# Performance work log

Hardware: AMD Instinct MI355X
Metric: run time of the kernel (lower is better)

Reference implementation:

```python
import jax, jax.numpy as jnp
import numpy as np


def crf_log_likelihood(logits, tags, mask, transitions, start_trans, end_trans):
    """AllenNLP-style linear-chain CRF log-likelihood, summed over the batch.
    logits: [B,T,K] float, tags: [B,T] int, mask: [B,T] float (1=valid).
    include_start_end_transitions=True.
    """
    B, T, K = logits.shape
    lt = jnp.transpose(logits, (1, 0, 2))          # [T,B,K]
    mt = jnp.transpose(mask, (1, 0))               # [T,B]
    tt = jnp.transpose(tags, (1, 0))               # [T,B]

    # ---- partition function (forward algorithm) ----
    alpha0 = start_trans + lt[0]                   # [B,K]

    def part_step(alpha, xs):
        emit, m = xs                               # emit [B,K], m [B]
        # inner[b,i,j] = alpha[b,i] + transitions[i,j] + emit[b,j]
        inner = alpha[:, :, None] + emit[:, None, :] + transitions[None, :, :]
        new_alpha = jax.nn.logsumexp(inner, axis=1)
        alpha = new_alpha * m[:, None] + alpha * (1.0 - m[:, None])
        return alpha, None

    alpha, _ = jax.lax.scan(part_step, alpha0, (lt[1:], mt[1:]))
    log_denominator = jax.nn.logsumexp(alpha + end_trans, axis=1)  # [B]

    # ---- joint (gold-path) score ----
    score0 = start_trans[tt[0]]                    # [B]

    def joint_step(score, xs):
        cur, nxt, emit, m_cur, m_nxt = xs
        trans_s = transitions[cur, nxt]                                   # [B]
        emit_s = jnp.take_along_axis(emit, cur[:, None], axis=1)[:, 0]    # [B]
        return score + trans_s * m_nxt + emit_s * m_cur, None

    score, _ = jax.lax.scan(joint_step, score0,
                            (tt[:-1], tt[1:], lt[:-1], mt[:-1], mt[1:]))
    last_idx = (jnp.sum(mt, axis=0) - 1.0).astype(jnp.int32)              # [B]
    last_tags = tt[last_idx, jnp.arange(B)]                               # [B]
    last_emit = jnp.take_along_axis(lt[-1], last_tags[:, None], axis=1)[:, 0]
    score = score + end_trans[last_tags] + last_emit * mt[-1]
    return jnp.sum(score - log_denominator)


def setup_inputs() -> dict:
    key = jax.random.key(0)
    ks = jax.random.split(key, 6)
    B, T, D, K = 64, 512, 768, 21
    vectors = jax.random.normal(ks[0], (B, T, D), dtype=jnp.float32)
    targets = jax.random.randint(ks[1], (B, T), 0, K, dtype=jnp.int32)
    mask = jnp.ones((B, T), dtype=jnp.int32)
    # Linear(input_dim, n_classes)
    W = jax.random.normal(ks[2], (K, D), dtype=jnp.float32) * (1.0 / np.sqrt(D))
    b = jax.random.normal(ks[3], (K,), dtype=jnp.float32) * 0.01
    transitions = jax.random.normal(ks[4], (K, K), dtype=jnp.float32) * 0.1
    se = jax.random.normal(ks[5], (2, K), dtype=jnp.float32) * 0.1
    return {"vectors": vectors, "targets": targets, "mask": mask,
            "W": W, "b": b, "transitions": transitions,
            "start_trans": se[0], "end_trans": se[1]}


def reference(vectors, targets, mask, W, b, transitions, start_trans, end_trans):
    logits = jnp.einsum('btd,kd->btk', vectors, W) + b     # proj
    maskf = mask.astype(logits.dtype)
    ll = crf_log_likelihood(logits, targets, maskf, transitions, start_trans, end_trans)
    loss = -ll / jnp.sum(maskf)
    return loss, logits
```

## Files before the change

### kernel.cpp

```cpp
#include <hip/hip_runtime.h>

#define B_ 64
#define T_ 512
#define D_ 768
#define K_ 21
#define NCHUNK 32
#define CLEN 16
#define GSTRIDE 448
#define LOG21 3.0445224377234229965f

using f16x8 = __attribute__((ext_vector_type(8))) _Float16;
using f32x4 = __attribute__((ext_vector_type(4))) float;

__global__ __launch_bounds__(256) void proj_kernel(
    const float* __restrict__ A,
    const float* __restrict__ W,
    const float* __restrict__ bias,
    float* __restrict__ out)
{
    const int lane = threadIdx.x & 63;
    const int wave = threadIdx.x >> 6;
    const int row0 = (blockIdx.x * 4 + wave) * 16;
    const int m = lane & 15;
    const int kb = (lane >> 4) * 8;

    const float* __restrict__ Ar  = A + (size_t)(row0 + m) * D_ + kb;
    const float* __restrict__ Wr0 = W + (size_t)m * D_ + kb;
    const int n1 = (16 + m < K_) ? 16 + m : K_ - 1;
    const float* __restrict__ Wr1 = W + (size_t)n1 * D_ + kb;

    f32x4 acc0 = {0.f, 0.f, 0.f, 0.f};
    f32x4 acc1 = {0.f, 0.f, 0.f, 0.f};

    #pragma unroll 8
    for (int s = 0; s < 24; ++s) {
        const float4 aL = *(const float4*)(Ar  + s * 32);
        const float4 aH = *(const float4*)(Ar  + s * 32 + 4);
        const float4 bL = *(const float4*)(Wr0 + s * 32);
        const float4 bH = *(const float4*)(Wr0 + s * 32 + 4);
        const float4 cL = *(const float4*)(Wr1 + s * 32);
        const float4 cH = *(const float4*)(Wr1 + s * 32 + 4);
        f16x8 af, bf, cf;
        af[0]=(_Float16)aL.x; af[1]=(_Float16)aL.y; af[2]=(_Float16)aL.z; af[3]=(_Float16)aL.w;
        af[4]=(_Float16)aH.x; af[5]=(_Float16)aH.y; af[6]=(_Float16)aH.z; af[7]=(_Float16)aH.w;
        bf[0]=(_Float16)bL.x; bf[1]=(_Float16)bL.y; bf[2]=(_Float16)bL.z; bf[3]=(_Float16)bL.w;
        bf[4]=(_Float16)bH.x; bf[5]=(_Float16)bH.y; bf[6]=(_Float16)bH.z; bf[7]=(_Float16)bH.w;
        cf[0]=(_Float16)cL.x; cf[1]=(_Float16)cL.y; cf[2]=(_Float16)cL.z; cf[3]=(_Float16)cL.w;
        cf[4]=(_Float16)cH.x; cf[5]=(_Float16)cH.y; cf[6]=(_Float16)cH.z; cf[7]=(_Float16)cH.w;
        acc0 = __builtin_amdgcn_mfma_f32_16x16x32_f16(af, bf, acc0, 0, 0, 0);
        acc1 = __builtin_amdgcn_mfma_f32_16x16x32_f16(af, cf, acc1, 0, 0, 0);
    }

    const int rbase = row0 + (lane >> 4) * 4;
    {
        const float bb = bias[m];
        float* o = out + 1 + (size_t)rbase * K_ + m;
        #pragma unroll
        for (int r = 0; r < 4; ++r) o[(size_t)r * K_] = acc0[r] + bb;
    }
    const int col2 = 16 + m;
    if (col2 < K_) {
        const float bb = bias[col2];
        float* o = out + 1 + (size_t)rbase * K_ + col2;
        #pragma unroll
        for (int r = 0; r < 4; ++r) o[(size_t)r * K_] = acc1[r] + bb;
    }
}

__global__ __launch_bounds__(64) void chunk_kernel(
    const float* __restrict__ outF,
    const int*   __restrict__ mask,
    const float* __restrict__ trans,
    float* __restrict__ G,
    float* __restrict__ SC)
{
    __shared__ float M0[441], M1[441];
    __shared__ float sET[441];
    __shared__ float em[CLEN * K_];
    __shared__ float smx[CLEN];
    __shared__ int   smask[CLEN];

    const int c = blockIdx.x;
    const int b = blockIdx.y;
    const int lane = threadIdx.x;
    const int t0 = c * CLEN + 1;
    const int nst = min(CLEN, T_ - t0);
    const int i_ = lane / 3;
    const int jg = lane - i_ * 3;
    const bool act = lane < 63;

    const float* lg = outF + 1 + (size_t)b * T_ * K_;
    for (int idx = lane; idx < nst * K_; idx += 64) em[idx] = lg[t0 * K_ + idx];
    if (lane < nst) smask[lane] = mask[b * T_ + t0 + lane];
    for (int idx = lane; idx < 441; idx += 64) {
        M0[idx] = (idx % 22 == 0) ? 1.0f : 0.0f;
        sET[idx] = __expf(trans[idx]);
    }
    __syncthreads();

    if (lane < nst) {
        float mx = -1e30f;
        for (int j = 0; j < K_; ++j) mx = fmaxf(mx, em[lane * K_ + j]);
        smx[lane] = mx;
    }
    __syncthreads();
    for (int idx = lane; idx < nst * K_; idx += 64)
        em[idx] = __expf(em[idx] - smx[idx / K_]) * (1.0f / 21.0f);

    float ETc[K_ * 7];
    if (act) {
        #pragma unroll
        for (int mm = 0; mm < K_; ++mm) {
            #pragma unroll
            for (int q = 0; q < 7; ++q)
                ETc[mm * 7 + q] = sET[mm * K_ + jg * 7 + q];
        }
    }
    __syncthreads();

    int cur = 0;
    for (int s = 0; s < nst; ++s) {
        if (smask[s] != 0) {
            const float* Mr = cur ? M1 : M0;
            float*       Mw = cur ? M0 : M1;
            float facc[7] = {0.f,0.f,0.f,0.f,0.f,0.f,0.f};
            if (act) {
                #pragma unroll
                for (int mm = 0; mm < K_; ++mm) {
                    const float lm = Mr[i_ * K_ + mm];
                    #pragma unroll
                    for (int q = 0; q < 7; ++q)
                        facc[q] = fmaf(lm, ETc[mm * 7 + q], facc[q]);
                }
            }
            __syncthreads();
            if (act) {
                #pragma unroll
                for (int q = 0; q < 7; ++q)
                    Mw[i_ * K_ + jg * 7 + q] = facc[q] * em[s * K_ + jg * 7 + q];
            }
            __syncthreads();
            cur ^= 1;
        }
    }

    float* Gc = G + (size_t)(b * NCHUNK + c) * GSTRIDE;
    const float* Mf = cur ? M1 : M0;
    for (int idx = lane; idx < 441; idx += 64) Gc[idx] = Mf[idx];
    if (lane == 0) {
        float sc = 0.0f;
        for (int s = 0; s < nst; ++s)
            if (smask[s] != 0) sc += smx[s] + LOG21;
        SC[b * NCHUNK + c] = sc;
    }
}

__global__ __launch_bounds__(64) void scan_kernel(
    const float* __restrict__ outF,
    const int*   __restrict__ tags,
    const int*   __restrict__ mask,
    const float* __restrict__ trans,
    const float* __restrict__ startT,
    const float* __restrict__ endT,
    const float* __restrict__ G,
    const float* __restrict__ SC,
    float* __restrict__ ll,
    float* __restrict__ msum)
{
    __shared__ float sG[NCHUNK * GSTRIDE];
    __shared__ float sv[24];
    __shared__ float sm[T_];
    __shared__ int   st[T_];
    const int b = blockIdx.x;
    const int lane = threadIdx.x;
    const int jc = min(lane, K_ - 1);
    const float* lg = outF + 1 + (size_t)b * T_ * K_;
    const float* Gb = G + (size_t)b * NCHUNK * GSTRIDE;

    {
        const float4* Gf4 = (const float4*)Gb;
        float4* dst = (float4*)sG;
        for (int j = lane; j < NCHUNK * GSTRIDE / 4; j += 64) dst[j] = Gf4[j];
    }
    for (int t = lane; t < T_; t += 64) {
        sm[t] = (float)mask[b * T_ + t];
        st[t] = tags[b * T_ + t];
    }
    const float scv = (lane < NCHUNK) ? SC[b * NCHUNK + lane] : 0.0f;

    float val = (lane < K_) ? startT[lane] + lg[lane] : -1e30f;
    float mx = val;
    #pragma unroll
    for (int off = 32; off >= 1; off >>= 1) mx = fmaxf(mx, __shfl_xor(mx, off, 64));
    float v = (lane < K_) ? __expf(val - mx) : 0.0f;
    float C = mx;
    __syncthreads();

    for (int c = 0; c < NCHUNK; ++c) {
        if (lane < K_) sv[lane] = v;
        __syncthreads();
        const float* Gc = sG + c * GSTRIDE;
        float a0 = 0.f, a1 = 0.f, a2 = 0.f;
        #pragma unroll
        for (int i = 0; i < K_; i += 3) {
            a0 = fmaf(sv[i],     Gc[i * K_ + jc],       a0);
            a1 = fmaf(sv[i + 1], Gc[(i + 1) * K_ + jc], a1);
            a2 = fmaf(sv[i + 2], Gc[(i + 2) * K_ + jc], a2);
        }
        const float s = a0 + a1 + a2;
        C += __shfl(scv, c, 64);
        float m2 = (lane < K_) ? s : 0.0f;
        #pragma unroll
        for (int off = 32; off >= 1; off >>= 1) m2 = fmaxf(m2, __shfl_xor(m2, off, 64));
        v = (lane < K_) ? s / m2 : 0.0f;
        C += __logf(m2);
        __syncthreads();
    }

    float term = (lane < K_) ? v * __expf(endT[lane]) : 0.0f;
    #pragma unroll
    for (int off = 32; off >= 1; off >>= 1) term += __shfl_xor(term, off, 64);
    const float logZ = C + __logf(term);

    float sc = 0.0f, ms = 0.0f;
    for (int t = lane; t < T_; t += 64) {
        const float mt = sm[t];
        ms += mt;
        if (t < T_ - 1) {
            const int ct = st[t], nt2 = st[t + 1];
            sc += trans[ct * K_ + nt2] * sm[t + 1] + lg[t * K_ + ct] * mt;
        }
    }
    #pragma unroll
    for (int off = 32; off >= 1; off >>= 1) {
        sc += __shfl_xor(sc, off, 64);
        ms += __shfl_xor(ms, off, 64);
    }
    if (lane == 0) {
        const int lastIdx = (int)ms - 1;
        const int lastTag = st[lastIdx];
        sc += startT[st[0]] + endT[lastTag] + lg[(T_ - 1) * K_ + lastTag] * sm[T_ - 1];
        ll[b]   = sc - logZ;
        msum[b] = ms;
    }
}

__global__ __launch_bounds__(64) void crf_kernel(
    const float* __restrict__ outF,
    const int*   __restrict__ tags,
    const int*   __restrict__ mask,
    const float* __restrict__ trans,
    const float* __restrict__ startT,
    const float* __restrict__ endT,
    float* __restrict__ ws)
{
    __shared__ float se[T_ * K_];
    __shared__ float sm[T_];
    __shared__ int   st[T_];
    const int b = blockIdx.x;
    const int lane = threadIdx.x;

    const float* lg = outF + 1 + (size_t)b * T_ * K_;
    for (int i = lane; i < T_ * K_; i += 64) se[i] = lg[i];
    for (int t = lane; t < T_; t += 64) {
        sm[t] = (float)mask[b * T_ + t];
        st[t] = tags[b * T_ + t];
    }
    __syncthreads();

    const int jc = lane < K_ ? lane : K_ - 1;
    float ET[K_];
    #pragma unroll
    for (int i = 0; i < K_; ++i) ET[i] = __expf(trans[i * K_ + jc]);

    float a0   = startT[jc] + se[jc];
    float r0   = __shfl(a0, 0, 64);
    float aRel = a0 - r0;
    float C    = r0;

    for (int t = 1; t < T_; ++t) {
        if (sm[t] != 0.0f) {
            float e = __expf(aRel);
            float s = 0.0f;
            #pragma unroll
            for (int i = 0; i < K_; ++i)
                s = fmaf(__shfl(e, i, 64), ET[i], s);
            float raw = __logf(s) + se[t * K_ + jc];
            float rr  = __shfl(raw, 0, 64);
            aRel = raw - rr;
            C   += rr;
        }
    }

    float contrib = (lane < K_) ? __expf(aRel + endT[jc]) : 0.0f;
    #pragma unroll
    for (int off = 32; off >= 1; off >>= 1) contrib += __shfl_xor(contrib, off, 64);
    const float logZ = C + __logf(contrib);

    float sc = 0.0f, ms = 0.0f;
    for (int t = lane; t < T_; t += 64) {
        const float mt = sm[t];
        ms += mt;
        if (t < T_ - 1) {
            const int ct = st[t], nt2 = st[t + 1];
            sc += trans[ct * K_ + nt2] * sm[t + 1] + se[t * K_ + ct] * mt;
        }
    }
    #pragma unroll
    for (int off = 32; off >= 1; off >>= 1) {
        sc += __shfl_xor(sc, off, 64);
        ms += __shfl_xor(ms, off, 64);
    }
    if (lane == 0) {
        const int lastIdx = (int)ms - 1;
        const int lastTag = st[lastIdx];
        sc += startT[st[0]] + endT[lastTag] + se[(T_ - 1) * K_ + lastTag] * sm[T_ - 1];
        ws[b]      = sc - logZ;
        ws[B_ + b] = ms;
    }
}

__global__ __launch_bounds__(64) void fin_kernel(
    const float* __restrict__ ll, const float* __restrict__ msum,
    float* __restrict__ outF)
{
    const int lane = threadIdx.x;
    float l = ll[lane];
    float m = msum[lane];
    #pragma unroll
    for (int off = 32; off >= 1; off >>= 1) {
        l += __shfl_xor(l, off, 64);
        m += __shfl_xor(m, off, 64);
    }
    if (lane == 0) outF[0] = -l / m;
}

extern "C" void kernel_launch(void* const* d_in, const int* in_sizes, int n_in,
                              void* d_out, int out_size, void* d_ws, size_t ws_size,
                              hipStream_t stream) {
    const float* A     = (const float*)d_in[0];
    const int*   tags  = (const int*)  d_in[1];
    const int*   mask  = (const int*)  d_in[2];
    const float* W     = (const float*)d_in[3];
    const float* bias  = (const float*)d_in[4];
    const float* trans = (const float*)d_in[5];
    const float* stT   = (const float*)d_in[6];
    const float* enT   = (const float*)d_in[7];
    float* outF = (float*)d_out;
    float* ws   = (float*)d_ws;

    proj_kernel<<<512, 256, 0, stream>>>(A, W, bias, outF);

    const size_t gFloats  = (size_t)B_ * NCHUNK * GSTRIDE;
    const size_t scOff    = gFloats;
    const size_t llOff    = gFloats + (size_t)B_ * NCHUNK;
    const size_t msOff    = llOff + B_;
    const size_t needBytes = (msOff + B_) * sizeof(float);

    if (ws_size >= needBytes) {
        float* G   = ws;
        float* SC  = ws + scOff;
        float* llp = ws + llOff;
        float* msv = ws + msOff;
        chunk_kernel<<<dim3(NCHUNK, B_), 64, 0, stream>>>(outF, mask, trans, G, SC);
        scan_kernel<<<B_, 64, 0, stream>>>(outF, tags, mask, trans, stT, enT, G, SC, llp, msv);
        fin_kernel<<<1, 64, 0, stream>>>(llp, msv, outF);
    } else {
        crf_kernel<<<B_, 64, 0, stream>>>(outF, tags, mask, trans, stT, enT, ws);
        fin_kernel<<<1, 64, 0, stream>>>(ws, ws + B_, outF);
    }
}
```

Baseline: 225.9 us.

## Fuse projection GEMM with per-chunk CRF transfer-matrix products in one kernel

```diff
diff --git a/kernel.cpp b/kernel.cpp
--- a/kernel.cpp
+++ b/kernel.cpp
@@ -5,24 +5,40 @@
 #define D_ 768
 #define K_ 21
 #define NCHUNK 32
-#define CLEN 16
 #define GSTRIDE 448
 #define LOG21 3.0445224377234229965f
 
 using f16x8 = __attribute__((ext_vector_type(8))) _Float16;
 using f32x4 = __attribute__((ext_vector_type(4))) float;
 
-__global__ __launch_bounds__(256) void proj_kernel(
+__global__ __launch_bounds__(256) void proj_chunk_kernel(
     const float* __restrict__ A,
     const float* __restrict__ W,
     const float* __restrict__ bias,
-    float* __restrict__ out)
+    const int*   __restrict__ mask,
+    const float* __restrict__ trans,
+    float* __restrict__ out,
+    float* __restrict__ G,
+    float* __restrict__ SC)
 {
-    const int lane = threadIdx.x & 63;
-    const int wave = threadIdx.x >> 6;
-    const int row0 = (blockIdx.x * 4 + wave) * 16;
-    const int m = lane & 15;
-    const int kb = (lane >> 4) * 8;
+    __shared__ float sET[441];
+    __shared__ float em[4][16 * K_];
+    __shared__ float smx[4][16];
+    __shared__ int   smk[4][16];
+    __shared__ float M[4][2][441];
+
+    const int tid  = threadIdx.x;
+    const int lane = tid & 63;
+    const int w    = tid >> 6;
+    const int blk  = blockIdx.x;
+    const int b    = blk >> 3;
+    const int j    = blk & 7;
+    const int row0 = blk * 64 + w * 16;
+    const int m    = lane & 15;
+    const int quad = lane >> 4;
+    const int kb   = quad * 8;
+
+    for (int idx = tid; idx < 441; idx += 256) sET[idx] = __expf(trans[idx]);
 
     const float* __restrict__ Ar  = A + (size_t)(row0 + m) * D_ + kb;
     const float* __restrict__ Wr0 = W + (size_t)m * D_ + kb;
@@ -32,7 +48,7 @@
     f32x4 acc0 = {0.f, 0.f, 0.f, 0.f};
     f32x4 acc1 = {0.f, 0.f, 0.f, 0.f};
 
-    #pragma unroll 8
+    #pragma unroll 2
     for (int s = 0; s < 24; ++s) {
         const float4 aL = *(const float4*)(Ar  + s * 32);
         const float4 aH = *(const float4*)(Ar  + s * 32 + 4);
@@ -51,62 +67,47 @@
         acc1 = __builtin_amdgcn_mfma_f32_16x16x32_f16(af, cf, acc1, 0, 0, 0);
     }
 
-    const int rbase = row0 + (lane >> 4) * 4;
+    const int rloc = quad * 4;
     {
         const float bb = bias[m];
-        float* o = out + 1 + (size_t)rbase * K_ + m;
-        #pragma unroll
-        for (int r = 0; r < 4; ++r) o[(size_t)r * K_] = acc0[r] + bb;
+        float* o = out + 1 + (size_t)(row0 + rloc) * K_ + m;
+        #pragma unroll
+        for (int r = 0; r < 4; ++r) {
+            const float v = acc0[r] + bb;
+            o[(size_t)r * K_] = v;
+            em[w][(rloc + r) * K_ + m] = v;
+        }
     }
     const int col2 = 16 + m;
     if (col2 < K_) {
         const float bb = bias[col2];
-        float* o = out + 1 + (size_t)rbase * K_ + col2;
-        #pragma unroll
-        for (int r = 0; r < 4; ++r) o[(size_t)r * K_] = acc1[r] + bb;
-    }
-}
-
-__global__ __launch_bounds__(64) void chunk_kernel(
-    const float* __restrict__ outF,
-    const int*   __restrict__ mask,
-    const float* __restrict__ trans,
-    float* __restrict__ G,
-    float* __restrict__ SC)
-{
-    __shared__ float M0[441], M1[441];
-    __shared__ float sET[441];
-    __shared__ float em[CLEN * K_];
-    __shared__ float smx[CLEN];
-    __shared__ int   smask[CLEN];
-
-    const int c = blockIdx.x;
-    const int b = blockIdx.y;
-    const int lane = threadIdx.x;
-    const int t0 = c * CLEN + 1;
-    const int nst = min(CLEN, T_ - t0);
+        float* o = out + 1 + (size_t)(row0 + rloc) * K_ + col2;
+        #pragma unroll
+        for (int r = 0; r < 4; ++r) {
+            const float v = acc1[r] + bb;
+            o[(size_t)r * K_] = v;
+            em[w][(rloc + r) * K_ + col2] = v;
+        }
+    }
+    if (lane < 16) smk[w][lane] = mask[b * T_ + j * 64 + w * 16 + lane];
+    __syncthreads();
+
+    if (lane < 16) {
+        float mx = -1e30f;
+        #pragma unroll
+        for (int c = 0; c < K_; ++c) mx = fmaxf(mx, em[w][lane * K_ + c]);
+        smx[w][lane] = mx;
+    }
+    __syncthreads();
+
+    for (int idx = lane; idx < 16 * K_; idx += 64)
+        em[w][idx] = __expf(em[w][idx] - smx[w][idx / K_]) * (1.0f / 21.0f);
+    for (int idx = lane; idx < 441; idx += 64)
+        M[w][0][idx] = (idx % 22 == 0) ? 1.0f : 0.0f;
+
     const int i_ = lane / 3;
     const int jg = lane - i_ * 3;
     const bool act = lane < 63;
-
-    const float* lg = outF + 1 + (size_t)b * T_ * K_;
-    for (int idx = lane; idx < nst * K_; idx += 64) em[idx] = lg[t0 * K_ + idx];
-    if (lane < nst) smask[lane] = mask[b * T_ + t0 + lane];
-    for (int idx = lane; idx < 441; idx += 64) {
-        M0[idx] = (idx % 22 == 0) ? 1.0f : 0.0f;
-        sET[idx] = __expf(trans[idx]);
-    }
-    __syncthreads();
-
-    if (lane < nst) {
-        float mx = -1e30f;
-        for (int j = 0; j < K_; ++j) mx = fmaxf(mx, em[lane * K_ + j]);
-        smx[lane] = mx;
-    }
-    __syncthreads();
-    for (int idx = lane; idx < nst * K_; idx += 64)
-        em[idx] = __expf(em[idx] - smx[idx / K_]) * (1.0f / 21.0f);
-
     float ETc[K_ * 7];
     if (act) {
         #pragma unroll
@@ -118,13 +119,16 @@
     }
     __syncthreads();
 
+    volatile float* Mv0 = M[w][0];
+    volatile float* Mv1 = M[w][1];
     int cur = 0;
-    for (int s = 0; s < nst; ++s) {
-        if (smask[s] != 0) {
-            const float* Mr = cur ? M1 : M0;
-            float*       Mw = cur ? M0 : M1;
-            float facc[7] = {0.f,0.f,0.f,0.f,0.f,0.f,0.f};
+    const int startS = (j == 0 && w == 0) ? 1 : 0;
+    for (int sI = startS; sI < 16; ++sI) {
+        if (smk[w][sI] != 0) {
+            volatile float* Mr = cur ? Mv1 : Mv0;
+            float*          Mw = cur ? M[w][0] : M[w][1];
             if (act) {
+                float facc[7] = {0.f,0.f,0.f,0.f,0.f,0.f,0.f};
                 #pragma unroll
                 for (int mm = 0; mm < K_; ++mm) {
                     const float lm = Mr[i_ * K_ + mm];
@@ -132,26 +136,22 @@
                     for (int q = 0; q < 7; ++q)
                         facc[q] = fmaf(lm, ETc[mm * 7 + q], facc[q]);
                 }
-            }
-            __syncthreads();
-            if (act) {
                 #pragma unroll
                 for (int q = 0; q < 7; ++q)
-                    Mw[i_ * K_ + jg * 7 + q] = facc[q] * em[s * K_ + jg * 7 + q];
+                    Mw[i_ * K_ + jg * 7 + q] = facc[q] * em[w][sI * K_ + jg * 7 + q];
             }
-            __syncthreads();
             cur ^= 1;
         }
     }
 
-    float* Gc = G + (size_t)(b * NCHUNK + c) * GSTRIDE;
-    const float* Mf = cur ? M1 : M0;
+    volatile float* Mf = cur ? Mv1 : Mv0;
+    float* Gc = G + (size_t)(b * NCHUNK + j * 4 + w) * GSTRIDE;
     for (int idx = lane; idx < 441; idx += 64) Gc[idx] = Mf[idx];
     if (lane == 0) {
         float sc = 0.0f;
-        for (int s = 0; s < nst; ++s)
-            if (smask[s] != 0) sc += smx[s] + LOG21;
-        SC[b * NCHUNK + c] = sc;
+        for (int sI = startS; sI < 16; ++sI)
+            if (smk[w][sI] != 0) sc += smx[w][sI] + LOG21;
+        SC[b * NCHUNK + j * 4 + w] = sc;
     }
 }
 
@@ -180,7 +180,7 @@
     {
         const float4* Gf4 = (const float4*)Gb;
         float4* dst = (float4*)sG;
-        for (int j = lane; j < NCHUNK * GSTRIDE / 4; j += 64) dst[j] = Gf4[j];
+        for (int i = lane; i < NCHUNK * GSTRIDE / 4; i += 64) dst[i] = Gf4[i];
     }
     for (int t = lane; t < T_; t += 64) {
         sm[t] = (float)mask[b * T_ + t];
@@ -242,6 +242,76 @@
         sc += startT[st[0]] + endT[lastTag] + lg[(T_ - 1) * K_ + lastTag] * sm[T_ - 1];
         ll[b]   = sc - logZ;
         msum[b] = ms;
+    }
+}
+
+__global__ __launch_bounds__(64) void fin_kernel(
+    const float* __restrict__ ll, const float* __restrict__ msum,
+    float* __restrict__ outF)
+{
+    const int lane = threadIdx.x;
+    float l = ll[lane];
+    float m = msum[lane];
+    #pragma unroll
+    for (int off = 32; off >= 1; off >>= 1) {
+        l += __shfl_xor(l, off, 64);
+        m += __shfl_xor(m, off, 64);
+    }
+    if (lane == 0) outF[0] = -l / m;
+}
+
+__global__ __launch_bounds__(256) void proj_kernel(
+    const float* __restrict__ A,
+    const float* __restrict__ W,
+    const float* __restrict__ bias,
+    float* __restrict__ out)
+{
+    const int lane = threadIdx.x & 63;
+    const int wave = threadIdx.x >> 6;
+    const int row0 = (blockIdx.x * 4 + wave) * 16;
+    const int m = lane & 15;
+    const int kb = (lane >> 4) * 8;
+
+    const float* __restrict__ Ar  = A + (size_t)(row0 + m) * D_ + kb;
+    const float* __restrict__ Wr0 = W + (size_t)m * D_ + kb;
+    const int n1 = (16 + m < K_) ? 16 + m : K_ - 1;
+    const float* __restrict__ Wr1 = W + (size_t)n1 * D_ + kb;
+
+    f32x4 acc0 = {0.f, 0.f, 0.f, 0.f};
+    f32x4 acc1 = {0.f, 0.f, 0.f, 0.f};
+
+    #pragma unroll 2
+    for (int s = 0; s < 24; ++s) {
+        const float4 aL = *(const float4*)(Ar  + s * 32);
+        const float4 aH = *(const float4*)(Ar  + s * 32 + 4);
+        const float4 bL = *(const float4*)(Wr0 + s * 32);
+        const float4 bH = *(const float4*)(Wr0 + s * 32 + 4);
+        const float4 cL = *(const float4*)(Wr1 + s * 32);
+        const float4 cH = *(const float4*)(Wr1 + s * 32 + 4);
+        f16x8 af, bf, cf;
+        af[0]=(_Float16)aL.x; af[1]=(_Float16)aL.y; af[2]=(_Float16)aL.z; af[3]=(_Float16)aL.w;
+        af[4]=(_Float16)aH.x; af[5]=(_Float16)aH.y; af[6]=(_Float16)aH.z; af[7]=(_Float16)aH.w;
+        bf[0]=(_Float16)bL.x; bf[1]=(_Float16)bL.y; bf[2]=(_Float16)bL.z; bf[3]=(_Float16)bL.w;
+        bf[4]=(_Float16)bH.x; bf[5]=(_Float16)bH.y; bf[6]=(_Float16)bH.z; bf[7]=(_Float16)bH.w;
+        cf[0]=(_Float16)cL.x; cf[1]=(_Float16)cL.y; cf[2]=(_Float16)cL.z; cf[3]=(_Float16)cL.w;
+        cf[4]=(_Float16)cH.x; cf[5]=(_Float16)cH.y; cf[6]=(_Float16)cH.z; cf[7]=(_Float16)cH.w;
+        acc0 = __builtin_amdgcn_mfma_f32_16x16x32_f16(af, bf, acc0, 0, 0, 0);
+        acc1 = __builtin_amdgcn_mfma_f32_16x16x32_f16(af, cf, acc1, 0, 0, 0);
+    }
+
+    const int rbase = row0 + (lane >> 4) * 4;
+    {
+        const float bb = bias[m];
+        float* o = out + 1 + (size_t)rbase * K_ + m;
+        #pragma unroll
+        for (int r = 0; r < 4; ++r) o[(size_t)r * K_] = acc0[r] + bb;
+    }
+    const int col2 = 16 + m;
+    if (col2 < K_) {
+        const float bb = bias[col2];
+        float* o = out + 1 + (size_t)rbase * K_ + col2;
+        #pragma unroll
+        for (int r = 0; r < 4; ++r) o[(size_t)r * K_] = acc1[r] + bb;
     }
 }
 
@@ -320,21 +390,6 @@
     }
 }
 
-__global__ __launch_bounds__(64) void fin_kernel(
-    const float* __restrict__ ll, const float* __restrict__ msum,
-    float* __restrict__ outF)
-{
-    const int lane = threadIdx.x;
-    float l = ll[lane];
-    float m = msum[lane];
-    #pragma unroll
-    for (int off = 32; off >= 1; off >>= 1) {
-        l += __shfl_xor(l, off, 64);
-        m += __shfl_xor(m, off, 64);
-    }
-    if (lane == 0) outF[0] = -l / m;
-}
-
 extern "C" void kernel_launch(void* const* d_in, const int* in_sizes, int n_in,
                               void* d_out, int out_size, void* d_ws, size_t ws_size,
                               hipStream_t stream) {
@@ -349,8 +404,6 @@
     float* outF = (float*)d_out;
     float* ws   = (float*)d_ws;
 
-    proj_kernel<<<512, 256, 0, stream>>>(A, W, bias, outF);
-
     const size_t gFloats  = (size_t)B_ * NCHUNK * GSTRIDE;
     const size_t scOff    = gFloats;
     const size_t llOff    = gFloats + (size_t)B_ * NCHUNK;
@@ -362,10 +415,11 @@
         float* SC  = ws + scOff;
         float* llp = ws + llOff;
         float* msv = ws + msOff;
-        chunk_kernel<<<dim3(NCHUNK, B_), 64, 0, stream>>>(outF, mask, trans, G, SC);
+        proj_chunk_kernel<<<512, 256, 0, stream>>>(A, W, bias, mask, trans, outF, G, SC);
         scan_kernel<<<B_, 64, 0, stream>>>(outF, tags, mask, trans, stT, enT, G, SC, llp, msv);
         fin_kernel<<<1, 64, 0, stream>>>(llp, msv, outF);
     } else {
+        proj_kernel<<<512, 256, 0, stream>>>(A, W, bias, outF);
         crf_kernel<<<B_, 64, 0, stream>>>(outF, tags, mask, trans, stT, enT, ws);
         fin_kernel<<<1, 64, 0, stream>>>(ws, ws + B_, outF);
     }
```

After: 225.7 us. No clear change (-0.1%).

## Stage fp16 A/W tiles in LDS for projection and parallelize CRF scan kernel

Applied to the files above, without the earlier changes.

```diff
diff --git a/kernel.cpp b/kernel.cpp
--- a/kernel.cpp
+++ b/kernel.cpp
@@ -8,8 +8,11 @@
 #define CLEN 16
 #define GSTRIDE 448
 #define LOG21 3.0445224377234229965f
+#define WSTRIDE 776
+#define ASTRIDE 136
 
 using f16x8 = __attribute__((ext_vector_type(8))) _Float16;
+using h16x4 = __attribute__((ext_vector_type(4))) _Float16;
 using f32x4 = __attribute__((ext_vector_type(4))) float;
 
 __global__ __launch_bounds__(256) void proj_kernel(
@@ -18,56 +21,101 @@
     const float* __restrict__ bias,
     float* __restrict__ out)
 {
-    const int lane = threadIdx.x & 63;
-    const int wave = threadIdx.x >> 6;
-    const int row0 = (blockIdx.x * 4 + wave) * 16;
-    const int m = lane & 15;
-    const int kb = (lane >> 4) * 8;
-
-    const float* __restrict__ Ar  = A + (size_t)(row0 + m) * D_ + kb;
-    const float* __restrict__ Wr0 = W + (size_t)m * D_ + kb;
-    const int n1 = (16 + m < K_) ? 16 + m : K_ - 1;
-    const float* __restrict__ Wr1 = W + (size_t)n1 * D_ + kb;
+    __shared__ _Float16 Wh[K_ * WSTRIDE];
+    __shared__ _Float16 Ah[2][64 * ASTRIDE];
+    const int tid  = threadIdx.x;
+    const int lane = tid & 63;
+    const int w    = tid >> 6;
+    const int m    = lane & 15;
+    const int quad = lane >> 4;
+    const size_t row0 = (size_t)blockIdx.x * 64;
+
+    {
+        const float4* Wg = (const float4*)W;
+        for (int i = tid; i < K_ * D_ / 4; i += 256) {
+            const float4 v = Wg[i];
+            const int fi = i * 4;
+            const int r = fi / D_;
+            const int c = fi - r * D_;
+            h16x4 h;
+            h[0] = (_Float16)v.x; h[1] = (_Float16)v.y;
+            h[2] = (_Float16)v.z; h[3] = (_Float16)v.w;
+            *(h16x4*)(&Wh[r * WSTRIDE + c]) = h;
+        }
+    }
+
+    float4 pf[8];
+    #pragma unroll
+    for (int j = 0; j < 8; ++j) {
+        const int i = tid + j * 256;
+        const int r = i >> 5, c4 = i & 31;
+        pf[j] = *(const float4*)(A + (row0 + r) * D_ + c4 * 4);
+    }
+    #pragma unroll
+    for (int j = 0; j < 8; ++j) {
+        const int i = tid + j * 256;
+        const int r = i >> 5, c4 = i & 31;
+        h16x4 h;
+        h[0] = (_Float16)pf[j].x; h[1] = (_Float16)pf[j].y;
+        h[2] = (_Float16)pf[j].z; h[3] = (_Float16)pf[j].w;
+        *(h16x4*)(&Ah[0][r * ASTRIDE + c4 * 4]) = h;
+    }
+    __syncthreads();
 
     f32x4 acc0 = {0.f, 0.f, 0.f, 0.f};
     f32x4 acc1 = {0.f, 0.f, 0.f, 0.f};
-
-    #pragma unroll 8
-    for (int s = 0; s < 24; ++s) {
-        const float4 aL = *(const float4*)(Ar  + s * 32);
-        const float4 aH = *(const float4*)(Ar  + s * 32 + 4);
-        const float4 bL = *(const float4*)(Wr0 + s * 32);
-        const float4 bH = *(const float4*)(Wr0 + s * 32 + 4);
-        const float4 cL = *(const float4*)(Wr1 + s * 32);
-        const float4 cH = *(const float4*)(Wr1 + s * 32 + 4);
-        f16x8 af, bf, cf;
-        af[0]=(_Float16)aL.x; af[1]=(_Float16)aL.y; af[2]=(_Float16)aL.z; af[3]=(_Float16)aL.w;
-        af[4]=(_Float16)aH.x; af[5]=(_Float16)aH.y; af[6]=(_Float16)aH.z; af[7]=(_Float16)aH.w;
-        bf[0]=(_Float16)bL.x; bf[1]=(_Float16)bL.y; bf[2]=(_Float16)bL.z; bf[3]=(_Float16)bL.w;
-        bf[4]=(_Float16)bH.x; bf[5]=(_Float16)bH.y; bf[6]=(_Float16)bH.z; bf[7]=(_Float16)bH.w;
-        cf[0]=(_Float16)cL.x; cf[1]=(_Float16)cL.y; cf[2]=(_Float16)cL.z; cf[3]=(_Float16)cL.w;
-        cf[4]=(_Float16)cH.x; cf[5]=(_Float16)cH.y; cf[6]=(_Float16)cH.z; cf[7]=(_Float16)cH.w;
-        acc0 = __builtin_amdgcn_mfma_f32_16x16x32_f16(af, bf, acc0, 0, 0, 0);
-        acc1 = __builtin_amdgcn_mfma_f32_16x16x32_f16(af, cf, acc1, 0, 0, 0);
-    }
-
-    const int rbase = row0 + (lane >> 4) * 4;
+    const int n1 = (16 + m < K_) ? 16 + m : K_ - 1;
+
+    for (int kt = 0; kt < 6; ++kt) {
+        if (kt < 5) {
+            #pragma unroll
+            for (int j = 0; j < 8; ++j) {
+                const int i = tid + j * 256;
+                const int r = i >> 5, c4 = i & 31;
+                pf[j] = *(const float4*)(A + (row0 + r) * D_ + (kt + 1) * 128 + c4 * 4);
+            }
+        }
+        const _Float16* Ab = Ah[kt & 1];
+        #pragma unroll
+        for (int s = 0; s < 4; ++s) {
+            const f16x8 af = *(const f16x8*)(&Ab[(w * 16 + m) * ASTRIDE + s * 32 + quad * 8]);
+            const f16x8 bf = *(const f16x8*)(&Wh[m * WSTRIDE + kt * 128 + s * 32 + quad * 8]);
+            const f16x8 cf = *(const f16x8*)(&Wh[n1 * WSTRIDE + kt * 128 + s * 32 + quad * 8]);
+            acc0 = __builtin_amdgcn_mfma_f32_16x16x32_f16(af, bf, acc0, 0, 0, 0);
+            acc1 = __builtin_amdgcn_mfma_f32_16x16x32_f16(af, cf, acc1, 0, 0, 0);
+        }
+        if (kt < 5) {
+            _Float16* Aw = Ah[(kt + 1) & 1];
+            #pragma unroll
+            for (int j = 0; j < 8; ++j) {
+                const int i = tid + j * 256;
+                const int r = i >> 5, c4 = i & 31;
+                h16x4 h;
+                h[0] = (_Float16)pf[j].x; h[1] = (_Float16)pf[j].y;
+                h[2] = (_Float16)pf[j].z; h[3] = (_Float16)pf[j].w;
+                *(h16x4*)(&Aw[r * ASTRIDE + c4 * 4]) = h;
+            }
+        }
+        __syncthreads();
+    }
+
+    const size_t rbase = row0 + w * 16 + quad * 4;
     {
         const float bb = bias[m];
-        float* o = out + 1 + (size_t)rbase * K_ + m;
+        float* o = out + 1 + rbase * K_ + m;
         #pragma unroll
         for (int r = 0; r < 4; ++r) o[(size_t)r * K_] = acc0[r] + bb;
     }
     const int col2 = 16 + m;
     if (col2 < K_) {
         const float bb = bias[col2];
-        float* o = out + 1 + (size_t)rbase * K_ + col2;
+        float* o = out + 1 + rbase * K_ + col2;
         #pragma unroll
         for (int r = 0; r < 4; ++r) o[(size_t)r * K_] = acc1[r] + bb;
     }
 }
 
-__global__ __launch_bounds__(64) void chunk_kernel(
+__global__ __launch_bounds__(64, 1) void chunk_kernel(
     const float* __restrict__ outF,
     const int*   __restrict__ mask,
     const float* __restrict__ trans,
@@ -155,7 +203,7 @@
     }
 }
 
-__global__ __launch_bounds__(64) void scan_kernel(
+__global__ __launch_bounds__(256) void scan_kernel(
     const float* __restrict__ outF,
     const int*   __restrict__ tags,
     const int*   __restrict__ mask,
@@ -168,81 +216,94 @@
     float* __restrict__ msum)
 {
     __shared__ float sG[NCHUNK * GSTRIDE];
-    __shared__ float sv[24];
     __shared__ float sm[T_];
     __shared__ int   st[T_];
+    __shared__ float part[8];
+    const int tid = threadIdx.x;
+    const int lane = tid & 63;
+    const int w = tid >> 6;
     const int b = blockIdx.x;
-    const int lane = threadIdx.x;
-    const int jc = min(lane, K_ - 1);
     const float* lg = outF + 1 + (size_t)b * T_ * K_;
-    const float* Gb = G + (size_t)b * NCHUNK * GSTRIDE;
 
     {
-        const float4* Gf4 = (const float4*)Gb;
+        const float4* Gf4 = (const float4*)(G + (size_t)b * NCHUNK * GSTRIDE);
         float4* dst = (float4*)sG;
-        for (int j = lane; j < NCHUNK * GSTRIDE / 4; j += 64) dst[j] = Gf4[j];
-    }
-    for (int t = lane; t < T_; t += 64) {
+        for (int i = tid; i < NCHUNK * GSTRIDE / 4; i += 256) dst[i] = Gf4[i];
+    }
+    for (int t = tid; t < T_; t += 256) {
         sm[t] = (float)mask[b * T_ + t];
         st[t] = tags[b * T_ + t];
     }
-    const float scv = (lane < NCHUNK) ? SC[b * NCHUNK + lane] : 0.0f;
-
-    float val = (lane < K_) ? startT[lane] + lg[lane] : -1e30f;
-    float mx = val;
-    #pragma unroll
-    for (int off = 32; off >= 1; off >>= 1) mx = fmaxf(mx, __shfl_xor(mx, off, 64));
-    float v = (lane < K_) ? __expf(val - mx) : 0.0f;
-    float C = mx;
-    __syncthreads();
-
-    for (int c = 0; c < NCHUNK; ++c) {
-        if (lane < K_) sv[lane] = v;
-        __syncthreads();
-        const float* Gc = sG + c * GSTRIDE;
-        float a0 = 0.f, a1 = 0.f, a2 = 0.f;
-        #pragma unroll
-        for (int i = 0; i < K_; i += 3) {
-            a0 = fmaf(sv[i],     Gc[i * K_ + jc],       a0);
-            a1 = fmaf(sv[i + 1], Gc[(i + 1) * K_ + jc], a1);
-            a2 = fmaf(sv[i + 2], Gc[(i + 2) * K_ + jc], a2);
-        }
-        const float s = a0 + a1 + a2;
-        C += __shfl(scv, c, 64);
-        float m2 = (lane < K_) ? s : 0.0f;
-        #pragma unroll
-        for (int off = 32; off >= 1; off >>= 1) m2 = fmaxf(m2, __shfl_xor(m2, off, 64));
-        v = (lane < K_) ? s / m2 : 0.0f;
-        C += __logf(m2);
-        __syncthreads();
-    }
-
-    float term = (lane < K_) ? v * __expf(endT[lane]) : 0.0f;
-    #pragma unroll
-    for (int off = 32; off >= 1; off >>= 1) term += __shfl_xor(term, off, 64);
-    const float logZ = C + __logf(term);
-
-    float sc = 0.0f, ms = 0.0f;
-    for (int t = lane; t < T_; t += 64) {
-        const float mt = sm[t];
-        ms += mt;
-        if (t < T_ - 1) {
-            const int ct = st[t], nt2 = st[t + 1];
-            sc += trans[ct * K_ + nt2] * sm[t + 1] + lg[t * K_ + ct] * mt;
-        }
-    }
-    #pragma unroll
-    for (int off = 32; off >= 1; off >>= 1) {
-        sc += __shfl_xor(sc, off, 64);
-        ms += __shfl_xor(ms, off, 64);
-    }
-    if (lane == 0) {
+    __syncthreads();
+
+    float logZ = 0.0f;
+    if (w == 0) {
+        const float scv = (lane < NCHUNK) ? SC[b * NCHUNK + lane] : 0.0f;
+        const int jc = min(lane, K_ - 1);
+        float v = (lane < K_) ? __expf(startT[lane] + lg[lane]) : 0.0f;
+        float C = 0.0f;
+        for (int c = 0; c < NCHUNK; ++c) {
+            const float* Gc = sG + c * GSTRIDE;
+            float a0 = 0.f, a1 = 0.f, a2 = 0.f;
+            #pragma unroll
+            for (int i = 0; i < K_; i += 3) {
+                a0 = fmaf(__shfl(v, i,     64), Gc[i * K_ + jc],       a0);
+                a1 = fmaf(__shfl(v, i + 1, 64), Gc[(i + 1) * K_ + jc], a1);
+                a2 = fmaf(__shfl(v, i + 2, 64), Gc[(i + 2) * K_ + jc], a2);
+            }
+            const float s = a0 + a1 + a2;
+            const float s0 = __shfl(s, 0, 64);
+            v = s / s0;
+            C += __logf(s0) + __shfl(scv, c, 64);
+        }
+        float term = (lane < K_) ? v * __expf(endT[lane]) : 0.0f;
+        #pragma unroll
+        for (int off = 16; off >= 1; off >>= 1) term += __shfl_xor(term, off, 64);
+        term += __shfl_xor(term, 32, 64);
+        logZ = C + __logf(term);
+    } else {
+        float sc = 0.0f, ms = 0.0f;
+        for (int t = tid - 64; t < T_; t += 192) {
+            const float mt = sm[t];
+            ms += mt;
+            if (t < T_ - 1) {
+                const int ct = st[t], nt2 = st[t + 1];
+                sc += trans[ct * K_ + nt2] * sm[t + 1] + lg[t * K_ + ct] * mt;
+            }
+        }
+        #pragma unroll
+        for (int off = 32; off >= 1; off >>= 1) {
+            sc += __shfl_xor(sc, off, 64);
+            ms += __shfl_xor(ms, off, 64);
+        }
+        if (lane == 0) { part[w] = sc; part[4 + w] = ms; }
+    }
+    __syncthreads();
+
+    if (tid == 0) {
+        float sc = part[1] + part[2] + part[3];
+        float ms = part[5] + part[6] + part[7];
         const int lastIdx = (int)ms - 1;
         const int lastTag = st[lastIdx];
         sc += startT[st[0]] + endT[lastTag] + lg[(T_ - 1) * K_ + lastTag] * sm[T_ - 1];
         ll[b]   = sc - logZ;
         msum[b] = ms;
     }
+}
+
+__global__ __launch_bounds__(64) void fin_kernel(
+    const float* __restrict__ ll, const float* __restrict__ msum,
+    float* __restrict__ outF)
+{
+    const int lane = threadIdx.x;
+    float l = ll[lane];
+    float m = msum[lane];
+    #pragma unroll
+    for (int off = 32; off >= 1; off >>= 1) {
+        l += __shfl_xor(l, off, 64);
+        m += __shfl_xor(m, off, 64);
+    }
+    if (lane == 0) outF[0] = -l / m;
 }
 
 __global__ __launch_bounds__(64) void crf_kernel(
@@ -320,21 +381,6 @@
     }
 }
 
-__global__ __launch_bounds__(64) void fin_kernel(
-    const float* __restrict__ ll, const float* __restrict__ msum,
-    float* __restrict__ outF)
-{
-    const int lane = threadIdx.x;
-    float l = ll[lane];
-    float m = msum[lane];
-    #pragma unroll
-    for (int off = 32; off >= 1; off >>= 1) {
-        l += __shfl_xor(l, off, 64);
-        m += __shfl_xor(m, off, 64);
-    }
-    if (lane == 0) outF[0] = -l / m;
-}
-
 extern "C" void kernel_launch(void* const* d_in, const int* in_sizes, int n_in,
                               void* d_out, int out_size, void* d_ws, size_t ws_size,
                               hipStream_t stream) {
@@ -363,7 +409,7 @@
         float* llp = ws + llOff;
         float* msv = ws + msOff;
         chunk_kernel<<<dim3(NCHUNK, B_), 64, 0, stream>>>(outF, mask, trans, G, SC);
-        scan_kernel<<<B_, 64, 0, stream>>>(outF, tags, mask, trans, stT, enT, G, SC, llp, msv);
+        scan_kernel<<<B_, 256, 0, stream>>>(outF, tags, mask, trans, stT, enT, G, SC, llp, msv);
         fin_kernel<<<1, 64, 0, stream>>>(llp, msv, outF);
     } else {
         crf_kernel<<<B_, 64, 0, stream>>>(outF, tags, mask, trans, stT, enT, ws);
```

Result: faster. 206.4 us (-8.6%).
